# Kernel tuning notes

Measured on AMD Instinct MI355X. Metric: run time of the kernel, lower is better.

The kernel has to match this reference:

```python
import jax, jax.numpy as jnp
import numpy as np

B, C, T = 4, 256, 4096
EPS = 1e-5
NEG = -1e8


def setup_inputs() -> dict:
    key = jax.random.key(0)
    ks = jax.random.split(key, 12)
    s = 1.0 / np.sqrt(C)
    x = jax.random.normal(ks[0], (B, C, T), dtype=jnp.float32)
    x_mask = (jax.random.uniform(ks[1], (B, 1, T)) > 0.1).astype(jnp.float32)
    return {
        "x": x,
        "x_mask": x_mask,
        # Normalize params
        "gamma": jnp.ones((C,), jnp.float32),
        "beta": jnp.zeros((C,), jnp.float32),
        "Wp": jax.random.normal(ks[2], (C, C), jnp.float32) * s,
        "bp": jnp.zeros((C,), jnp.float32),
        # 1x1 conv projections (weight [C_out, C_in])
        "Wq": jax.random.normal(ks[3], (C, C), jnp.float32) * s,
        "bq": jnp.zeros((C,), jnp.float32),
        "Wk": jax.random.normal(ks[4], (C, C), jnp.float32) * s,
        "bk": jnp.zeros((C,), jnp.float32),
        "Wv": jax.random.normal(ks[5], (C, C), jnp.float32) * s,
        "bv": jnp.zeros((C,), jnp.float32),
        "Wo": jax.random.normal(ks[6], (C, C), jnp.float32) * s,
        "bo": jnp.zeros((C,), jnp.float32),
    }


def _conv1x1(W, b, x):
    # x: [B, C, T] -> [B, C, T]
    return jnp.einsum('oc,bct->bot', W, x) + b[None, :, None]


def reference(x, x_mask, gamma, beta, Wp, bp, Wq, bq, Wk, bk, Wv, bv, Wo, bo):
    m = x_mask  # [B,1,T]
    h = x * m
    # Normalize: layer_norm over channel dim + linear, operating on [B,T,C]
    ht = h.transpose(0, 2, 1)  # [B,T,C]
    mu = jnp.mean(ht, axis=-1, keepdims=True)
    var = jnp.mean(jnp.square(ht - mu), axis=-1, keepdims=True)
    ln = (ht - mu) * jax.lax.rsqrt(var + EPS) * gamma + beta
    ln = ln @ Wp.T + bp
    h = ln.transpose(0, 2, 1) * m  # [B,C,T]

    q = _conv1x1(Wq, bq, h) * m
    k = _conv1x1(Wk, bk, h) * m
    v = _conv1x1(Wv, bv, h) * m

    scale = float(C) ** (-0.5)
    # scores[b,t,s] = sum_c q[b,c,t] k[b,c,s]
    w = jnp.einsum('bct,bcs->bts', q, k) * scale
    neg = (1.0 - m) * NEG  # [B,1,T]
    w = w + neg + neg.transpose(0, 2, 1)  # mask keys and queries
    w = jax.nn.softmax(w, axis=2)
    # h_[b,c,t] = sum_s v[b,c,s] w[b,t,s]
    h = jnp.einsum('bcs,bts->bct', v, w)
    h = _conv1x1(Wo, bo, h) * m
    return (x + h) * m
```

## Files before the change

### kernel.cpp

```cpp
#include <hip/hip_runtime.h>

#define Bn 4
#define Cn 256
#define Tn 4096

typedef unsigned short u16;
typedef __bf16 bf16x8 __attribute__((ext_vector_type(8)));
typedef float f32x4 __attribute__((ext_vector_type(4)));
typedef float f32x16 __attribute__((ext_vector_type(16)));
typedef u16 u16x8 __attribute__((ext_vector_type(8)));

__device__ __forceinline__ float b2f(u16 u) {
    union { unsigned int i; float f; } v;
    v.i = ((unsigned int)u) << 16;
    return v.f;
}
__device__ __forceinline__ u16 f2b(float f) {
    union { float f; unsigned int i; } v;
    v.f = f;
    unsigned int r = v.i + 0x7FFFu + ((v.i >> 16) & 1u);
    return (u16)(r >> 16);
}
__device__ __forceinline__ bf16x8 ones8() {
    union { u16 u[8]; bf16x8 v; } t;
    for (int j = 0; j < 8; j++) t.u[j] = 0x3F80;
    return t.v;
}

__global__ __launch_bounds__(256) void cvt_kernel(
    const float* __restrict__ w0, const float* __restrict__ w1,
    const float* __restrict__ w2, const float* __restrict__ w3,
    const float* __restrict__ w4, u16* __restrict__ dst)
{
    int gid = blockIdx.x * 256 + threadIdx.x;
    int base = gid * 4;
    int region = base >> 16;
    int off = base & 65535;
    const float* src = region == 0 ? w0 : region == 1 ? w1
                     : region == 2 ? w2 : region == 3 ? w3 : w4;
    float4 v = *(const float4*)(src + off);
    ushort4 o;
    o.x = f2b(v.x); o.y = f2b(v.y); o.z = f2b(v.z); o.w = f2b(v.w);
    *(ushort4*)(dst + base) = o;
}

__global__ __launch_bounds__(256) void ln_kernel(
    const float* __restrict__ x, const float* __restrict__ mask,
    const float* __restrict__ gamma, const float* __restrict__ beta,
    u16* __restrict__ lnT)
{
    __shared__ __attribute__((aligned(16))) u16 tile[32][264];
    __shared__ float ssum[8][32], ssq[8][32], smu[32], srs[32];
    const int tid = threadIdx.x;
    const int b = blockIdx.y;
    const int t0 = blockIdx.x * 32;
    const int g = tid >> 5, tl = tid & 31;
    const int t = t0 + tl;
    const float mval = mask[b * Tn + t];
    float s = 0.f, s2 = 0.f;
    for (int c = g; c < Cn; c += 8) {
        float v = x[((size_t)(b * Cn + c)) * Tn + t] * mval;
        s += v; s2 += v * v;
        tile[tl][c] = f2b(v);
    }
    ssum[g][tl] = s; ssq[g][tl] = s2;
    __syncthreads();
    if (tid < 32) {
        float su = 0.f, sq = 0.f;
        for (int k = 0; k < 8; k++) { su += ssum[k][tid]; sq += ssq[k][tid]; }
        float mu = su * (1.f / Cn);
        float var = sq * (1.f / Cn) - mu * mu;
        var = fmaxf(var, 0.0f);
        smu[tid] = mu;
        srs[tid] = 1.0f / sqrtf(var + 1e-5f);
    }
    __syncthreads();
    for (int it = 0; it < 4; it++) {
        int idx = it * 256 + tid;
        int row = idx >> 5, c16 = idx & 31;
        float mu = smu[row], rs = srs[row];
        u16x8 ov;
        for (int j = 0; j < 8; j++) {
            int c = c16 * 8 + j;
            float h = b2f(tile[row][c]);
            float v = (h - mu) * rs * gamma[c] + beta[c];
            ov[j] = f2b(v);
        }
        *(u16x8*)(lnT + ((size_t)(b * Tn + t0 + row)) * Cn + c16 * 8) = ov;
    }
}

template<bool ORIENT2, bool FINAL, bool FUSE2>
__global__ __launch_bounds__(256) void gemm_kernel(
    const u16* __restrict__ Xb,
    const u16* __restrict__ Wb,  const float* __restrict__ bias,
    const u16* __restrict__ Wb2, const float* __restrict__ bias2,
    const float* __restrict__ mask,
    const float* __restrict__ xres,
    u16* __restrict__ Yout, u16* __restrict__ Yout2,
    float* __restrict__ YoutF)
{
    __shared__ __attribute__((aligned(16))) u16 Al[128][72];
    __shared__ __attribute__((aligned(16))) u16 Bl[64][72];
    const int tid = threadIdx.x;
    int b, which = 0;
    if (FUSE2) { which = blockIdx.z >= Bn; b = blockIdx.z - which * Bn; }
    else b = blockIdx.z;
    const u16* W = (FUSE2 && which) ? Wb2 : Wb;
    const float* bi = (FUSE2 && which) ? bias2 : bias;
    u16* Yo = (FUSE2 && which) ? Yout2 : Yout;
    const int m0 = blockIdx.x * 128;
    const int n0 = blockIdx.y * 64;
    const int wave = tid >> 6, lane = tid & 63;
    const int ln16 = lane & 15, quad = lane >> 4;
    const int wm = (wave & 1) * 64, wn = (wave >> 1) * 32;

    const u16* Abase = ORIENT2 ? (W + (size_t)m0 * Cn)
                               : (Xb + ((size_t)(b * Tn + m0)) * Cn);
    const u16* Bbase = ORIENT2 ? (Xb + ((size_t)(b * Tn + n0)) * Cn)
                               : (W + (size_t)n0 * Cn);

    f32x4 acc[4][2];
    for (int i = 0; i < 4; i++)
        for (int j = 0; j < 2; j++) acc[i][j] = (f32x4){0.f, 0.f, 0.f, 0.f};

    for (int k0 = 0; k0 < Cn; k0 += 64) {
        for (int it = 0; it < 4; it++) {
            int idx = it * 256 + tid;
            int row = idx >> 3, gg = idx & 7;
            *(uint4*)(&Al[row][gg * 8]) =
                *(const uint4*)(Abase + (size_t)row * Cn + k0 + gg * 8);
        }
        for (int it = 0; it < 2; it++) {
            int idx = it * 256 + tid;
            int row = idx >> 3, gg = idx & 7;
            *(uint4*)(&Bl[row][gg * 8]) =
                *(const uint4*)(Bbase + (size_t)row * Cn + k0 + gg * 8);
        }
        __syncthreads();
        for (int kk = 0; kk < 2; kk++) {
            bf16x8 af[4], bfr[2];
            for (int i = 0; i < 4; i++)
                af[i] = *(const bf16x8*)(&Al[wm + i * 16 + ln16][kk * 32 + quad * 8]);
            for (int j = 0; j < 2; j++)
                bfr[j] = *(const bf16x8*)(&Bl[wn + j * 16 + ln16][kk * 32 + quad * 8]);
            for (int i = 0; i < 4; i++)
                for (int j = 0; j < 2; j++)
                    acc[i][j] = __builtin_amdgcn_mfma_f32_16x16x32_bf16(
                        af[i], bfr[j], acc[i][j], 0, 0, 0);
        }
        __syncthreads();
    }
    for (int i = 0; i < 4; i++) {
        for (int j = 0; j < 2; j++) {
            int mm = m0 + wm + i * 16 + quad * 4;
            int nn = n0 + wn + j * 16 + ln16;
            for (int r = 0; r < 4; r++) {
                int m = mm + r;
                float val = acc[i][j][r];
                if (!ORIENT2) {
                    int tt = m, oo = nn;
                    val += bi[oo];
                    val *= mask[b * Tn + tt];
                    Yo[((size_t)(b * Tn + tt)) * Cn + oo] = f2b(val);
                } else {
                    int oo = m, tt = nn;
                    val += bi[oo];
                    float mk = mask[b * Tn + tt];
                    if (FINAL) {
                        float xr = xres[((size_t)(b * Cn + oo)) * Tn + tt];
                        YoutF[((size_t)(b * Cn + oo)) * Tn + tt] = (xr + val * mk) * mk;
                    } else {
                        Yo[((size_t)(b * Cn + oo)) * Tn + tt] = f2b(val * mk);
                    }
                }
            }
        }
    }
}

__global__ __launch_bounds__(512, 2) void attn_kernel(
    const u16* __restrict__ qT, const u16* __restrict__ kT,
    const u16* __restrict__ vv, const float* __restrict__ mask,
    u16* __restrict__ PO, float* __restrict__ pL)
{
    __shared__ __attribute__((aligned(16))) u16 kls[32][264];
    __shared__ __attribute__((aligned(16))) u16 vls[256][40];
    __shared__ __attribute__((aligned(16))) u16 pls[8][32][40];
    __shared__ float nls[1024];
    const int tid = threadIdx.x;
    const int id = blockIdx.x;
    const int spl = id & 3;
    const int b = (id >> 2) & 3;
    const int qb = id >> 4;
    const int t0 = qb * 256;
    const int wave = tid >> 6, lane = tid & 63;
    const int ln32 = lane & 31, half = lane >> 5;
    const int sBeg = spl * (Tn / 4);

    for (int i = tid; i < 1024; i += 512)
        nls[i] = (1.0f - mask[b * Tn + sBeg + i]) * -1e8f - 8.0f;

    bf16x8 qf[16];
    {
        const u16* qp = qT + ((size_t)(b * Tn + t0 + wave * 32 + ln32)) * Cn + half * 8;
        for (int ks = 0; ks < 16; ks++) qf[ks] = *(const bf16x8*)(qp + ks * 16);
    }
    f32x16 acc[8], lac;
    for (int i = 0; i < 16; i++) lac[i] = 0.f;
    for (int nt = 0; nt < 8; nt++) acc[nt] = lac;
    const bf16x8 ones = ones8();

    const int nIter = (Tn / 4) / 32;

    uint4 kpre[2], vpre[2];
    auto loadK = [&](int s0) {
        for (int i = 0; i < 2; i++) {
            int idx = i * 512 + tid;
            kpre[i] = *(const uint4*)(kT + ((size_t)(b * Tn + s0 + (idx >> 5))) * Cn + (idx & 31) * 8);
        }
    };
    auto loadV = [&](int s0) {
        for (int i = 0; i < 2; i++) {
            int idx = i * 512 + tid;
            vpre[i] = *(const uint4*)(vv + ((size_t)(b * Cn + (idx >> 2))) * Tn + s0 + (idx & 3) * 8);
        }
    };
    loadK(sBeg);
    loadV(sBeg);

    for (int it = 0; it < nIter; it++) {
        const int s0 = sBeg + it * 32;
        __syncthreads();
        for (int i = 0; i < 2; i++) {
            int idx = i * 512 + tid;
            *(uint4*)(&kls[idx >> 5][(idx & 31) * 8]) = kpre[i];
        }
        for (int i = 0; i < 2; i++) {
            int idx = i * 512 + tid;
            *(uint4*)(&vls[idx >> 2][(idx & 3) * 8]) = vpre[i];
        }
        if (it + 1 < nIter) {
            loadK(s0 + 32);
            loadV(s0 + 32);
        }
        __syncthreads();
        const float negk = nls[it * 32 + ln32];

        f32x16 S;
        for (int i = 0; i < 16; i++) S[i] = 0.f;
        for (int ks = 0; ks < 16; ks++) {
            bf16x8 kf = *(const bf16x8*)(&kls[ln32][ks * 16 + half * 8]);
            S = __builtin_amdgcn_mfma_f32_32x32x16_bf16(qf[ks], kf, S, 0, 0, 0);
        }
        for (int r = 0; r < 16; r++) S[r] = __expf(S[r] * 0.0625f + negk);
        for (int r = 0; r < 16; r++) {
            int row = (r & 3) + 8 * (r >> 2) + 4 * half;
            pls[wave][row][ln32] = f2b(S[r]);
        }
        bf16x8 pf0 = *(const bf16x8*)(&pls[wave][ln32][half * 8]);
        bf16x8 pf1 = *(const bf16x8*)(&pls[wave][ln32][16 + half * 8]);
        lac = __builtin_amdgcn_mfma_f32_32x32x16_bf16(pf0, ones, lac, 0, 0, 0);
        lac = __builtin_amdgcn_mfma_f32_32x32x16_bf16(pf1, ones, lac, 0, 0, 0);
        for (int nt = 0; nt < 8; nt++) {
            bf16x8 v0 = *(const bf16x8*)(&vls[nt * 32 + ln32][half * 8]);
            bf16x8 v1 = *(const bf16x8*)(&vls[nt * 32 + ln32][16 + half * 8]);
            acc[nt] = __builtin_amdgcn_mfma_f32_32x32x16_bf16(pf0, v0, acc[nt], 0, 0, 0);
            acc[nt] = __builtin_amdgcn_mfma_f32_32x32x16_bf16(pf1, v1, acc[nt], 0, 0, 0);
        }
    }
    const size_t SB = (size_t)spl * (Bn * Tn);
    for (int r = 0; r < 16; r++) {
        int trow = (r & 3) + 8 * (r >> 2) + 4 * half;
        int t = t0 + wave * 32 + trow;
        for (int nt = 0; nt < 8; nt++)
            PO[(SB + b * Tn + t) * Cn + nt * 32 + ln32] = f2b(acc[nt][r]);
        if (ln32 == 0) pL[SB + b * Tn + t] = lac[r];
    }
}

__global__ __launch_bounds__(256) void combine_kernel(
    const u16* __restrict__ PO, const float* __restrict__ pL,
    u16* __restrict__ h2T)
{
    const int tid = threadIdx.x;
    const int c8 = (tid & 31) * 8;
    const int rsub = tid >> 5;
    const size_t BT = (size_t)Bn * Tn;
    for (int itr = 0; itr < 8; itr++) {
        const size_t R = (size_t)blockIdx.x * 64 + itr * 8 + rsub;
        float l = pL[R] + pL[BT + R] + pL[2 * BT + R] + pL[3 * BT + R];
        float rl = 1.0f / fmaxf(l, 1e-30f);
        u16x8 a0 = *(const u16x8*)(PO + R * Cn + c8);
        u16x8 a1 = *(const u16x8*)(PO + (BT + R) * Cn + c8);
        u16x8 a2 = *(const u16x8*)(PO + (2 * BT + R) * Cn + c8);
        u16x8 a3 = *(const u16x8*)(PO + (3 * BT + R) * Cn + c8);
        u16x8 o;
        for (int j = 0; j < 8; j++)
            o[j] = f2b((b2f(a0[j]) + b2f(a1[j]) + b2f(a2[j]) + b2f(a3[j])) * rl);
        *(u16x8*)(h2T + R * Cn + c8) = o;
    }
}

extern "C" void kernel_launch(void* const* d_in, const int* in_sizes, int n_in,
                              void* d_out, int out_size, void* d_ws, size_t ws_size,
                              hipStream_t stream)
{
    const float* x     = (const float*)d_in[0];
    const float* xmask = (const float*)d_in[1];
    const float* gamma = (const float*)d_in[2];
    const float* beta  = (const float*)d_in[3];
    const float* Wp = (const float*)d_in[4];
    const float* bp = (const float*)d_in[5];
    const float* Wq = (const float*)d_in[6];
    const float* bq = (const float*)d_in[7];
    const float* Wk = (const float*)d_in[8];
    const float* bk = (const float*)d_in[9];
    const float* Wv = (const float*)d_in[10];
    const float* bv = (const float*)d_in[11];
    const float* Wo = (const float*)d_in[12];
    const float* bo = (const float*)d_in[13];
    float* out = (float*)d_out;

    u16* ws = (u16*)d_ws;
    const size_t SZ = (size_t)Bn * Tn * Cn;
    const size_t WSZ = (size_t)Cn * Cn;
    u16* lnT = ws;
    u16* h1T = ws + SZ;
    u16* qTt = ws + 2 * SZ;
    u16* kTt = ws + 3 * SZ;
    u16* vB  = ws + 4 * SZ;
    u16* h2T = ws;
    u16* wbf = ws + 5 * SZ;
    u16* PO  = ws + 5 * SZ + 5 * WSZ;
    float* pL = (float*)(PO + 4 * SZ);

    u16* WpB = wbf;
    u16* WqB = wbf + WSZ;
    u16* WkB = wbf + 2 * WSZ;
    u16* WvB = wbf + 3 * WSZ;
    u16* WoB = wbf + 4 * WSZ;

    dim3 blk(256);
    cvt_kernel<<<dim3(320), blk, 0, stream>>>(Wp, Wq, Wk, Wv, Wo, wbf);
    ln_kernel<<<dim3(Tn / 32, Bn), blk, 0, stream>>>(x, xmask, gamma, beta, lnT);
    gemm_kernel<false, false, false><<<dim3(Tn / 128, Cn / 64, Bn), blk, 0, stream>>>(
        lnT, WpB, bp, nullptr, nullptr, xmask, nullptr, h1T, nullptr, nullptr);
    gemm_kernel<false, false, true><<<dim3(Tn / 128, Cn / 64, 2 * Bn), blk, 0, stream>>>(
        h1T, WqB, bq, WkB, bk, xmask, nullptr, qTt, kTt, nullptr);
    gemm_kernel<true, false, false><<<dim3(Cn / 128, Tn / 64, Bn), blk, 0, stream>>>(
        h1T, WvB, bv, nullptr, nullptr, xmask, nullptr, vB, nullptr, nullptr);
    attn_kernel<<<dim3(256), dim3(512), 0, stream>>>(qTt, kTt, vB, xmask, PO, pL);
    combine_kernel<<<dim3(Bn * Tn / 64), blk, 0, stream>>>(PO, pL, h2T);
    gemm_kernel<true, true, false><<<dim3(Cn / 128, Tn / 64, Bn), blk, 0, stream>>>(
        h2T, WoB, bo, nullptr, nullptr, xmask, x, nullptr, nullptr, out);
}
```

Baseline: 273.0 us.

## Fuse Q/K/V projections, fold softmax scale into Wq, merge combine into output GEMM

The V projection joins the Q/K projection kernel in one launch, and V's transposed [C,T] layout is staged through shared memory for coalesced stores. The softmax scale of 1/16 is folded into the bf16 Wq weights and bq bias, which removes a multiply per score in the attention kernel. The split-K combine kernel is folded into the output projection GEMM: the four partial outputs are summed while loading the B tile, and the 1/l normalisation is applied in the epilogue. This cuts launches and a full write and read of the intermediate h2, at the cost of four times more global reads per B tile in the final GEMM and one extra bf16 rounding of the scaled weights.

```diff
diff --git a/kernel.cpp b/kernel.cpp
--- a/kernel.cpp
+++ b/kernel.cpp
@@ -38,9 +38,11 @@
     int off = base & 65535;
     const float* src = region == 0 ? w0 : region == 1 ? w1
                      : region == 2 ? w2 : region == 3 ? w3 : w4;
+    float sc = (region == 1) ? 0.0625f : 1.0f;
     float4 v = *(const float4*)(src + off);
     ushort4 o;
-    o.x = f2b(v.x); o.y = f2b(v.y); o.z = f2b(v.z); o.w = f2b(v.w);
+    o.x = f2b(v.x * sc); o.y = f2b(v.y * sc);
+    o.z = f2b(v.z * sc); o.w = f2b(v.w * sc);
     *(ushort4*)(dst + base) = o;
 }
 
@@ -90,35 +92,23 @@
     }
 }
 
-template<bool ORIENT2, bool FINAL, bool FUSE2>
-__global__ __launch_bounds__(256) void gemm_kernel(
-    const u16* __restrict__ Xb,
-    const u16* __restrict__ Wb,  const float* __restrict__ bias,
-    const u16* __restrict__ Wb2, const float* __restrict__ bias2,
-    const float* __restrict__ mask,
-    const float* __restrict__ xres,
-    u16* __restrict__ Yout, u16* __restrict__ Yout2,
-    float* __restrict__ YoutF)
+__global__ __launch_bounds__(256) void wp_kernel(
+    const u16* __restrict__ Xb, const u16* __restrict__ Wb,
+    const float* __restrict__ bias, const float* __restrict__ mask,
+    u16* __restrict__ Yout)
 {
     __shared__ __attribute__((aligned(16))) u16 Al[128][72];
     __shared__ __attribute__((aligned(16))) u16 Bl[64][72];
     const int tid = threadIdx.x;
-    int b, which = 0;
-    if (FUSE2) { which = blockIdx.z >= Bn; b = blockIdx.z - which * Bn; }
-    else b = blockIdx.z;
-    const u16* W = (FUSE2 && which) ? Wb2 : Wb;
-    const float* bi = (FUSE2 && which) ? bias2 : bias;
-    u16* Yo = (FUSE2 && which) ? Yout2 : Yout;
+    const int b = blockIdx.z;
     const int m0 = blockIdx.x * 128;
     const int n0 = blockIdx.y * 64;
     const int wave = tid >> 6, lane = tid & 63;
     const int ln16 = lane & 15, quad = lane >> 4;
     const int wm = (wave & 1) * 64, wn = (wave >> 1) * 32;
 
-    const u16* Abase = ORIENT2 ? (W + (size_t)m0 * Cn)
-                               : (Xb + ((size_t)(b * Tn + m0)) * Cn);
-    const u16* Bbase = ORIENT2 ? (Xb + ((size_t)(b * Tn + n0)) * Cn)
-                               : (W + (size_t)n0 * Cn);
+    const u16* Abase = Xb + ((size_t)(b * Tn + m0)) * Cn;
+    const u16* Bbase = Wb + (size_t)n0 * Cn;
 
     f32x4 acc[4][2];
     for (int i = 0; i < 4; i++)
@@ -153,28 +143,109 @@
     }
     for (int i = 0; i < 4; i++) {
         for (int j = 0; j < 2; j++) {
-            int mm = m0 + wm + i * 16 + quad * 4;
             int nn = n0 + wn + j * 16 + ln16;
             for (int r = 0; r < 4; r++) {
-                int m = mm + r;
-                float val = acc[i][j][r];
-                if (!ORIENT2) {
-                    int tt = m, oo = nn;
-                    val += bi[oo];
+                int tt = m0 + wm + i * 16 + quad * 4 + r;
+                float val = acc[i][j][r] + bias[nn];
+                val *= mask[b * Tn + tt];
+                Yout[((size_t)(b * Tn + tt)) * Cn + nn] = f2b(val);
+            }
+        }
+    }
+}
+
+__global__ __launch_bounds__(256) void qkv_kernel(
+    const u16* __restrict__ h1T,
+    const u16* __restrict__ Wq_, const float* __restrict__ bq_,
+    const u16* __restrict__ Wk_, const float* __restrict__ bk_,
+    const u16* __restrict__ Wv_, const float* __restrict__ bv_,
+    const float* __restrict__ mask,
+    u16* __restrict__ qO, u16* __restrict__ kO, u16* __restrict__ vO)
+{
+    __shared__ __attribute__((aligned(16))) u16 Al[128][72];
+    __shared__ __attribute__((aligned(16))) u16 Bl[64][72];
+    const int tid = threadIdx.x;
+    const int z = blockIdx.z;
+    const int which = z >> 2;
+    const int b = z & 3;
+    const u16* W = which == 0 ? Wq_ : which == 1 ? Wk_ : Wv_;
+    const float* bi = which == 0 ? bq_ : which == 1 ? bk_ : bv_;
+    const float bsc = which == 0 ? 0.0625f : 1.0f;
+    const int m0 = blockIdx.x * 128;
+    const int n0 = blockIdx.y * 64;
+    const int wave = tid >> 6, lane = tid & 63;
+    const int ln16 = lane & 15, quad = lane >> 4;
+    const int wm = (wave & 1) * 64, wn = (wave >> 1) * 32;
+
+    const u16* Abase = h1T + ((size_t)(b * Tn + m0)) * Cn;
+    const u16* Bbase = W + (size_t)n0 * Cn;
+
+    f32x4 acc[4][2];
+    for (int i = 0; i < 4; i++)
+        for (int j = 0; j < 2; j++) acc[i][j] = (f32x4){0.f, 0.f, 0.f, 0.f};
+
+    for (int k0 = 0; k0 < Cn; k0 += 64) {
+        for (int it = 0; it < 4; it++) {
+            int idx = it * 256 + tid;
+            int row = idx >> 3, gg = idx & 7;
+            *(uint4*)(&Al[row][gg * 8]) =
+                *(const uint4*)(Abase + (size_t)row * Cn + k0 + gg * 8);
+        }
+        for (int it = 0; it < 2; it++) {
+            int idx = it * 256 + tid;
+            int row = idx >> 3, gg = idx & 7;
+            *(uint4*)(&Bl[row][gg * 8]) =
+                *(const uint4*)(Bbase + (size_t)row * Cn + k0 + gg * 8);
+        }
+        __syncthreads();
+        for (int kk = 0; kk < 2; kk++) {
+            bf16x8 af[4], bfr[2];
+            for (int i = 0; i < 4; i++)
+                af[i] = *(const bf16x8*)(&Al[wm + i * 16 + ln16][kk * 32 + quad * 8]);
+            for (int j = 0; j < 2; j++)
+                bfr[j] = *(const bf16x8*)(&Bl[wn + j * 16 + ln16][kk * 32 + quad * 8]);
+            for (int i = 0; i < 4; i++)
+                for (int j = 0; j < 2; j++)
+                    acc[i][j] = __builtin_amdgcn_mfma_f32_16x16x32_bf16(
+                        af[i], bfr[j], acc[i][j], 0, 0, 0);
+        }
+        __syncthreads();
+    }
+
+    if (which < 2) {
+        u16* Yo = which == 0 ? qO : kO;
+        for (int i = 0; i < 4; i++) {
+            for (int j = 0; j < 2; j++) {
+                int nn = n0 + wn + j * 16 + ln16;
+                for (int r = 0; r < 4; r++) {
+                    int tt = m0 + wm + i * 16 + quad * 4 + r;
+                    float val = acc[i][j][r] + bi[nn] * bsc;
                     val *= mask[b * Tn + tt];
-                    Yo[((size_t)(b * Tn + tt)) * Cn + oo] = f2b(val);
-                } else {
-                    int oo = m, tt = nn;
-                    val += bi[oo];
-                    float mk = mask[b * Tn + tt];
-                    if (FINAL) {
-                        float xr = xres[((size_t)(b * Cn + oo)) * Tn + tt];
-                        YoutF[((size_t)(b * Cn + oo)) * Tn + tt] = (xr + val * mk) * mk;
-                    } else {
-                        Yo[((size_t)(b * Cn + oo)) * Tn + tt] = f2b(val * mk);
-                    }
+                    Yo[((size_t)(b * Tn + tt)) * Cn + nn] = f2b(val);
                 }
             }
+        }
+    } else {
+        u16* vt = &Al[0][0];
+        for (int i = 0; i < 4; i++) {
+            for (int j = 0; j < 2; j++) {
+                int nl = wn + j * 16 + ln16;
+                for (int r = 0; r < 4; r++) {
+                    int ml = wm + i * 16 + quad * 4 + r;
+                    int tt = m0 + ml;
+                    float val = acc[i][j][r] + bi[n0 + nl];
+                    val *= mask[b * Tn + tt];
+                    vt[nl * 136 + ml] = f2b(val);
+                }
+            }
+        }
+        __syncthreads();
+        for (int itc = 0; itc < 4; itc++) {
+            int cidx = itc * 256 + tid;
+            int row = cidx >> 4;
+            int ch = cidx & 15;
+            u16x8 ov = *(const u16x8*)(vt + row * 136 + ch * 8);
+            *(u16x8*)(vO + ((size_t)(b * Cn + n0 + row)) * Tn + m0 + ch * 8) = ov;
         }
     }
 }
@@ -253,7 +324,7 @@
             bf16x8 kf = *(const bf16x8*)(&kls[ln32][ks * 16 + half * 8]);
             S = __builtin_amdgcn_mfma_f32_32x32x16_bf16(qf[ks], kf, S, 0, 0, 0);
         }
-        for (int r = 0; r < 16; r++) S[r] = __expf(S[r] * 0.0625f + negk);
+        for (int r = 0; r < 16; r++) S[r] = __expf(S[r] + negk);
         for (int r = 0; r < 16; r++) {
             int row = (r & 3) + 8 * (r >> 2) + 4 * half;
             pls[wave][row][ln32] = f2b(S[r]);
@@ -279,26 +350,81 @@
     }
 }
 
-__global__ __launch_bounds__(256) void combine_kernel(
+__global__ __launch_bounds__(256) void final_kernel(
+    const u16* __restrict__ WoB, const float* __restrict__ bo,
     const u16* __restrict__ PO, const float* __restrict__ pL,
-    u16* __restrict__ h2T)
-{
+    const float* __restrict__ mask, const float* __restrict__ x,
+    float* __restrict__ out)
+{
+    __shared__ __attribute__((aligned(16))) u16 Al[128][72];
+    __shared__ __attribute__((aligned(16))) u16 Bl[64][72];
+    __shared__ float rls[64];
     const int tid = threadIdx.x;
-    const int c8 = (tid & 31) * 8;
-    const int rsub = tid >> 5;
+    const int b = blockIdx.z;
+    const int m0 = blockIdx.x * 128;
+    const int n0 = blockIdx.y * 64;
+    const int wave = tid >> 6, lane = tid & 63;
+    const int ln16 = lane & 15, quad = lane >> 4;
+    const int wm = (wave & 1) * 64, wn = (wave >> 1) * 32;
     const size_t BT = (size_t)Bn * Tn;
-    for (int itr = 0; itr < 8; itr++) {
-        const size_t R = (size_t)blockIdx.x * 64 + itr * 8 + rsub;
+
+    if (tid < 64) {
+        size_t R = (size_t)b * Tn + n0 + tid;
         float l = pL[R] + pL[BT + R] + pL[2 * BT + R] + pL[3 * BT + R];
-        float rl = 1.0f / fmaxf(l, 1e-30f);
-        u16x8 a0 = *(const u16x8*)(PO + R * Cn + c8);
-        u16x8 a1 = *(const u16x8*)(PO + (BT + R) * Cn + c8);
-        u16x8 a2 = *(const u16x8*)(PO + (2 * BT + R) * Cn + c8);
-        u16x8 a3 = *(const u16x8*)(PO + (3 * BT + R) * Cn + c8);
-        u16x8 o;
-        for (int j = 0; j < 8; j++)
-            o[j] = f2b((b2f(a0[j]) + b2f(a1[j]) + b2f(a2[j]) + b2f(a3[j])) * rl);
-        *(u16x8*)(h2T + R * Cn + c8) = o;
+        rls[tid] = 1.0f / fmaxf(l, 1e-30f);
+    }
+
+    f32x4 acc[4][2];
+    for (int i = 0; i < 4; i++)
+        for (int j = 0; j < 2; j++) acc[i][j] = (f32x4){0.f, 0.f, 0.f, 0.f};
+
+    for (int k0 = 0; k0 < Cn; k0 += 64) {
+        for (int it = 0; it < 4; it++) {
+            int idx = it * 256 + tid;
+            int row = idx >> 3, gg = idx & 7;
+            *(uint4*)(&Al[row][gg * 8]) =
+                *(const uint4*)(WoB + (size_t)(m0 + row) * Cn + k0 + gg * 8);
+        }
+        for (int it = 0; it < 2; it++) {
+            int idx = it * 256 + tid;
+            int row = idx >> 3, gg = idx & 7;
+            size_t base = ((size_t)b * Tn + n0 + row) * Cn + k0 + gg * 8;
+            u16x8 a0 = *(const u16x8*)(PO + base);
+            u16x8 a1 = *(const u16x8*)(PO + BT * Cn + base);
+            u16x8 a2 = *(const u16x8*)(PO + 2 * BT * Cn + base);
+            u16x8 a3 = *(const u16x8*)(PO + 3 * BT * Cn + base);
+            u16x8 o;
+            for (int j = 0; j < 8; j++)
+                o[j] = f2b(b2f(a0[j]) + b2f(a1[j]) + b2f(a2[j]) + b2f(a3[j]));
+            *(u16x8*)(&Bl[row][gg * 8]) = o;
+        }
+        __syncthreads();
+        for (int kk = 0; kk < 2; kk++) {
+            bf16x8 af[4], bfr[2];
+            for (int i = 0; i < 4; i++)
+                af[i] = *(const bf16x8*)(&Al[wm + i * 16 + ln16][kk * 32 + quad * 8]);
+            for (int j = 0; j < 2; j++)
+                bfr[j] = *(const bf16x8*)(&Bl[wn + j * 16 + ln16][kk * 32 + quad * 8]);
+            for (int i = 0; i < 4; i++)
+                for (int j = 0; j < 2; j++)
+                    acc[i][j] = __builtin_amdgcn_mfma_f32_16x16x32_bf16(
+                        af[i], bfr[j], acc[i][j], 0, 0, 0);
+        }
+        __syncthreads();
+    }
+    for (int i = 0; i < 4; i++) {
+        for (int j = 0; j < 2; j++) {
+            int nl = wn + j * 16 + ln16;
+            int tt = n0 + nl;
+            float rl = rls[nl];
+            float mk = mask[b * Tn + tt];
+            for (int r = 0; r < 4; r++) {
+                int oo = m0 + wm + i * 16 + quad * 4 + r;
+                float val = acc[i][j][r] * rl + bo[oo];
+                float xr = x[((size_t)(b * Cn + oo)) * Tn + tt];
+                out[((size_t)(b * Cn + oo)) * Tn + tt] = (xr + val * mk) * mk;
+            }
+        }
     }
 }
 
@@ -330,7 +456,6 @@
     u16* qTt = ws + 2 * SZ;
     u16* kTt = ws + 3 * SZ;
     u16* vB  = ws + 4 * SZ;
-    u16* h2T = ws;
     u16* wbf = ws + 5 * SZ;
     u16* PO  = ws + 5 * SZ + 5 * WSZ;
     float* pL = (float*)(PO + 4 * SZ);
@@ -344,14 +469,11 @@
     dim3 blk(256);
     cvt_kernel<<<dim3(320), blk, 0, stream>>>(Wp, Wq, Wk, Wv, Wo, wbf);
     ln_kernel<<<dim3(Tn / 32, Bn), blk, 0, stream>>>(x, xmask, gamma, beta, lnT);
-    gemm_kernel<false, false, false><<<dim3(Tn / 128, Cn / 64, Bn), blk, 0, stream>>>(
-        lnT, WpB, bp, nullptr, nullptr, xmask, nullptr, h1T, nullptr, nullptr);
-    gemm_kernel<false, false, true><<<dim3(Tn / 128, Cn / 64, 2 * Bn), blk, 0, stream>>>(
-        h1T, WqB, bq, WkB, bk, xmask, nullptr, qTt, kTt, nullptr);
-    gemm_kernel<true, false, false><<<dim3(Cn / 128, Tn / 64, Bn), blk, 0, stream>>>(
-        h1T, WvB, bv, nullptr, nullptr, xmask, nullptr, vB, nullptr, nullptr);
+    wp_kernel<<<dim3(Tn / 128, Cn / 64, Bn), blk, 0, stream>>>(
+        lnT, WpB, bp, xmask, h1T);
+    qkv_kernel<<<dim3(Tn / 128, Cn / 64, 3 * Bn), blk, 0, stream>>>(
+        h1T, WqB, bq, WkB, bk, WvB, bv, xmask, qTt, kTt, vB);
     attn_kernel<<<dim3(256), dim3(512), 0, stream>>>(qTt, kTt, vB, xmask, PO, pL);
-    combine_kernel<<<dim3(Bn * Tn / 64), blk, 0, stream>>>(PO, pL, h2T);
-    gemm_kernel<true, true, false><<<dim3(Cn / 128, Tn / 64, Bn), blk, 0, stream>>>(
-        h2T, WoB, bo, nullptr, nullptr, xmask, x, nullptr, nullptr, out);
-}
+    final_kernel<<<dim3(Cn / 128, Tn / 64, Bn), blk, 0, stream>>>(
+        WoB, bo, PO, pL, xmask, x, out);
+}
```

Result: no change. 268.4 us (-1.7%).
